# Kernel optimization log

Hardware: AMD Instinct MI355X
Metric: run time of the kernel (lower is better)

Reference implementation:

```python
import jax, jax.numpy as jnp
import numpy as np

B, C2, H, W = 4, 1024, 64, 64  # features have 2*input_dim channels
CH = C2 // 2                   # 512 = input_dim
HID = CH // 4                  # 128 = hidden_channels


def setup_inputs() -> dict:
    key = jax.random.key(0)
    ks = jax.random.split(key, 6)
    left = jax.random.normal(ks[0], (B, C2, H, W), dtype=jnp.float32)
    right = jax.random.normal(ks[1], (B, C2, H, W), dtype=jnp.float32)
    # 1x1 conv params (weight [out,in], bias [out]) for query/reference projections
    Wq = jax.random.normal(ks[2], (HID, CH), dtype=jnp.float32) * 0.02
    bq = jax.random.normal(ks[3], (HID,), dtype=jnp.float32) * 0.02
    Wk = jax.random.normal(ks[4], (HID, CH), dtype=jnp.float32) * 0.02
    bk = jax.random.normal(ks[5], (HID,), dtype=jnp.float32) * 0.02
    return {"left_features": left, "right_features": right, "Wq": Wq, "bq": bq, "Wk": Wk, "bk": bk}


def _co_attention(qf, rf, Wq, bq, Wk, bk):
    # 1x1 convs == per-pixel channel matmuls
    Q = jnp.einsum('bchw,oc->bohw', qf, Wq) + bq[None, :, None, None]   # [B,HID,H,W]
    K = jnp.einsum('bchw,oc->bohw', rf, Wk) + bk[None, :, None, None]   # [B,HID,H,W]
    b, c, h, w = Q.shape
    Kf = K.reshape(b, c, h * w)                                          # [B,HID,P]
    V = rf.reshape(rf.shape[0], rf.shape[1], h * w)                      # [B,CH,P]
    # attention_map: einsum('bcij,bckl->bijkl') then flatten (kl) == contract channels
    attn = jnp.einsum('bcij,bcp->bijp', Q, Kf)                           # [B,H,W,P]
    attn = jax.nn.softmax(attn, axis=3)
    return jnp.einsum('bijp,bcp->bcij', attn, V)                         # [B,CH,H,W]


def _homo(qf, rf):
    weights = jax.nn.softmax(qf - rf, axis=1)  # softmax over channels
    return rf * weights


def _get_both_differences(q, r, Wq, bq, Wk, bk):
    c = q.shape[1] // 2
    q_orig, q_trans = q[:, :c], q[:, c:]
    r_orig = r[:, :c]
    cross = _co_attention(q_orig, r_orig, Wq, bq, Wk, bk)
    reduce = _homo(q_orig, q_trans)
    return jnp.concatenate([q_orig, cross + reduce], axis=1)


def reference(left_features, right_features, Wq, bq, Wk, bk):
    left_out = _get_both_differences(left_features, right_features, Wq, bq, Wk, bk)
    right_out = _get_both_differences(right_features, left_features, Wq, bq, Wk, bk)
    return (left_out, right_out)
```

## Files before the change

kernel.cpp:

```cpp
#include <hip/hip_runtime.h>
#include <hip/hip_bf16.h>

#define NB 4
#define LOG2E 1.4426950408889634f

typedef unsigned short u16;
typedef __attribute__((ext_vector_type(8))) short bf16x8;
typedef __attribute__((ext_vector_type(4))) float f32x4;

static __device__ __forceinline__ float bf2f(u16 u) {
    union { float f; unsigned v; } x; x.v = ((unsigned)u) << 16; return x.f;
}
static __device__ __forceinline__ u16 f2bf(float f) {
    unsigned v = __builtin_bit_cast(unsigned, f);
    return (u16)((v + 0x7FFFu + ((v >> 16) & 1u)) >> 16);
}
static __device__ __forceinline__ void gload_lds16(const u16* g, u16* l) {
    __builtin_amdgcn_global_load_lds(
        (const __attribute__((address_space(1))) unsigned*)(const void*)g,
        (__attribute__((address_space(3))) unsigned*)(void*)l, 16, 0, 0);
}

__global__ void k_wcvt(const float* __restrict__ Wq, const float* __restrict__ Wk,
                       u16* __restrict__ Wbq, u16* __restrict__ Wbk) {
    int i = blockIdx.x * 1024 + threadIdx.x;
    Wbq[i] = f2bf(Wq[i]);
    Wbk[i] = f2bf(Wk[i]);
}

__global__ __launch_bounds__(256) void k_cvtf(
        const float* __restrict__ L, const float* __restrict__ R,
        u16* __restrict__ Lb, u16* __restrict__ Rb,
        u16* __restrict__ web, float* __restrict__ sumsH, float* __restrict__ out) {
    __shared__ float4 red[16][16];
    int idx = blockIdx.x;
    int sb = idx & 7, pblk = (idx >> 3) & 63, cpart = idx >> 9;
    int side = sb & 1, b = sb >> 1;
    int osb = side * 4 + b;
    const float* src = (side ? R : L) + (size_t)b * 1024 * 4096;
    int tid = threadIdx.x;
    int p4 = tid & 15, cg = tid >> 4;
    int p = pblk * 64 + p4 * 4;
    int cbase = cpart * 128 + cg * 8;
    const float* ao = src + (size_t)cbase * 4096 + p;
    const float* at = src + (size_t)(512 + cbase) * 4096 + p;
    u16* lbdst = (side ? Rb : Lb) + ((size_t)b * 512 + cbase) * 4096 + p;
    float* odst = out + ((size_t)osb * 1024 + cbase) * 4096 + p;
    u16* wdst = web + ((size_t)osb * 512 + cbase) * 4096 + p;
    float4 sm = {0.f, 0.f, 0.f, 0.f};
#pragma unroll
    for (int cc = 0; cc < 8; cc++) {
        float4 a = *reinterpret_cast<const float4*>(ao + (size_t)cc * 4096);
        float4 t = *reinterpret_cast<const float4*>(at + (size_t)cc * 4096);
        ushort4 ub;
        ub.x = f2bf(a.x); ub.y = f2bf(a.y); ub.z = f2bf(a.z); ub.w = f2bf(a.w);
        *reinterpret_cast<ushort4*>(lbdst + (size_t)cc * 4096) = ub;
        *reinterpret_cast<float4*>(odst + (size_t)cc * 4096) = a;
        float4 e;
        e.x = exp2f((a.x - t.x) * LOG2E);
        e.y = exp2f((a.y - t.y) * LOG2E);
        e.z = exp2f((a.z - t.z) * LOG2E);
        e.w = exp2f((a.w - t.w) * LOG2E);
        sm.x += e.x; sm.y += e.y; sm.z += e.z; sm.w += e.w;
        ushort4 wb_;
        wb_.x = f2bf(t.x * e.x); wb_.y = f2bf(t.y * e.y);
        wb_.z = f2bf(t.z * e.z); wb_.w = f2bf(t.w * e.w);
        *reinterpret_cast<ushort4*>(wdst + (size_t)cc * 4096) = wb_;
    }
    red[cg][p4] = sm;
    __syncthreads();
    if (tid < 16) {
        float4 tot = {0.f, 0.f, 0.f, 0.f};
#pragma unroll
        for (int gR = 0; gR < 16; gR++) {
            float4 v = red[gR][tid];
            tot.x += v.x; tot.y += v.y; tot.z += v.z; tot.w += v.w;
        }
        *reinterpret_cast<float4*>(
            sumsH + ((size_t)cpart * 8 + osb) * 4096 + pblk * 64 + tid * 4) = tot;
    }
}

__global__ void k_cvt(const float* __restrict__ L, const float* __restrict__ R,
                      u16* __restrict__ Lb, u16* __restrict__ Rb, float* __restrict__ out) {
    int i = blockIdx.x * 256 + threadIdx.x;
    int pq = i & 1023;
    int c = (i >> 10) & 511;
    int b = (i >> 19) & 3;
    int side = i >> 21;
    const float* src = (side ? R : L) + ((long)(b * 1024 + c) << 12) + (pq << 2);
    float4 v = *reinterpret_cast<const float4*>(src);
    ushort4 u;
    u.x = f2bf(v.x); u.y = f2bf(v.y); u.z = f2bf(v.z); u.w = f2bf(v.w);
    *reinterpret_cast<ushort4*>((side ? Rb : Lb) + ((long)(b * 512 + c) << 12) + (pq << 2)) = u;
    *reinterpret_cast<float4*>(out + ((long)(side * 4 + b) * 1024 + c) * 4096 + (pq << 2)) = v;
}

__global__ __launch_bounds__(256) void k_proj(
        const u16* __restrict__ Lb, const u16* __restrict__ Rb,
        const u16* __restrict__ Wbq, const u16* __restrict__ Wbk,
        const float* __restrict__ bq, const float* __restrict__ bk,
        u16* __restrict__ QL, u16* __restrict__ KL,
        u16* __restrict__ QR, u16* __restrict__ KR) {
    __shared__ u16 XT[2][64 * 40];
    int pj = blockIdx.x & 15, pt = blockIdx.x >> 4;
    int ty = pj >> 2, b = pj & 3;
    const u16* src; const u16* Wb; const float* bias; u16* dst;
    if (ty == 0)      { src = Lb; Wb = Wbq; bias = bq; dst = QL; }
    else if (ty == 1) { src = Rb; Wb = Wbk; bias = bk; dst = KL; }
    else if (ty == 2) { src = Rb; Wb = Wbq; bias = bq; dst = QR; }
    else              { src = Lb; Wb = Wbk; bias = bk; dst = KR; }
    const u16* X = src + (long)b * 512 * 4096 + pt * 64;
    int tid = threadIdx.x;
    int wv = __builtin_amdgcn_readfirstlane(tid >> 6);
    int lane = tid & 63, g = lane >> 4, li = lane & 15;

    f32x4 acc[8];
#pragma unroll
    for (int ob = 0; ob < 8; ob++)
#pragma unroll
        for (int r = 0; r < 4; r++) acc[ob][r] = bias[ob * 16 + g * 4 + r];

    int c_r = tid >> 3, j = tid & 7;
    bf16x8 gx = *reinterpret_cast<const bf16x8*>(X + (long)c_r * 4096 + j * 8);
#pragma unroll
    for (int k = 0; k < 8; k++) XT[0][(j * 8 + k) * 40 + c_r] = (u16)gx[k];
    __syncthreads();

    for (int cc = 0; cc < 16; cc++) {
        int buf = cc & 1;
        bf16x8 gn;
        if (cc < 15)
            gn = *reinterpret_cast<const bf16x8*>(X + (long)(cc * 32 + 32 + c_r) * 4096 + j * 8);
        bf16x8 xb = *reinterpret_cast<const bf16x8*>(&XT[buf][(wv * 16 + li) * 40 + g * 8]);
#pragma unroll
        for (int ob = 0; ob < 8; ob++) {
            bf16x8 aw = *reinterpret_cast<const bf16x8*>(Wb + (long)(ob * 16 + li) * 512 + cc * 32 + g * 8);
            acc[ob] = __builtin_amdgcn_mfma_f32_16x16x32_bf16(aw, xb, acc[ob], 0, 0, 0);
        }
        if (cc < 15) {
#pragma unroll
            for (int k = 0; k < 8; k++) XT[buf ^ 1][(j * 8 + k) * 40 + c_r] = (u16)gn[k];
        }
        __syncthreads();
    }
    u16* d = dst + ((long)b * 4096 + pt * 64 + wv * 16 + li) * 128;
#pragma unroll
    for (int ob = 0; ob < 8; ob++) {
        uint2 w;
        w.x = (unsigned)f2bf(acc[ob][0]) | ((unsigned)f2bf(acc[ob][1]) << 16);
        w.y = (unsigned)f2bf(acc[ob][2]) | ((unsigned)f2bf(acc[ob][3]) << 16);
        *reinterpret_cast<uint2*>(d + ob * 16 + g * 4) = w;
    }
}

__global__ __launch_bounds__(512, 4) void k_qk(
        const u16* __restrict__ QL, const u16* __restrict__ KL,
        const u16* __restrict__ QR, const u16* __restrict__ KR,
        u16* __restrict__ P, float* __restrict__ sums,
        int bd0, int bdMask, int bdShift) {
    __shared__ u16 Kl[2][8192];
    __shared__ u16 Ps[4096];
    __shared__ float sred[4][2][16];
    int bdl = (int)blockIdx.x & bdMask;
    int rest = (int)blockIdx.x >> bdShift;
    int qtile = rest & 63;
    int ph0 = rest >> 6;
    int bd = bd0 + bdl, dir = bd & 1, b = bd >> 1;
    const u16* Qt = (dir ? QR : QL) + (size_t)b * 4096 * 128;
    const u16* Kt = (dir ? KR : KL) + (size_t)b * 4096 * 128;
    u16* Pbd = P + ((size_t)bdl << 24);
    int q0 = qtile * 64;
    int tid = threadIdx.x;
    int wv = __builtin_amdgcn_readfirstlane(tid >> 6);
    int lane = tid & 63, g = lane >> 4, li = lane & 15;
    int qt = wv >> 1, phw = wv & 1;

#define STAGE_K(BUF, PT)                                                                   \
    {                                                                                      \
        _Pragma("unroll") for (int r0 = 0; r0 < 2; r0++) {                                 \
            int o = r0 * 8192 + tid * 16;                                                  \
            int row = o >> 8, w = o & 255;                                                 \
            int sw = (w ^ ((row & 7) << 4)) >> 1;                                          \
            gload_lds16(Kt + (((size_t)((PT) * 64 + row)) << 7) + sw,                      \
                        &Kl[BUF][r0 * 4096 + wv * 512]);                                   \
        }                                                                                  \
    }

    bf16x8 qf[4];
#pragma unroll
    for (int hc = 0; hc < 4; hc++)
        qf[hc] = *reinterpret_cast<const bf16x8*>(
            Qt + (size_t)(q0 + qt * 16 + li) * 128 + hc * 32 + g * 8);
    float psum = 0.f;
    STAGE_K(0, ph0 * 32)

    for (int tt = 0; tt < 32; tt++) {
        int pt = ph0 * 32 + tt;
        if (tt == 0) asm volatile("s_waitcnt vmcnt(0) lgkmcnt(0)\n\ts_barrier" ::: "memory");
        else         asm volatile("s_waitcnt vmcnt(1) lgkmcnt(0)\n\ts_barrier" ::: "memory");
        if (tt < 31) STAGE_K((tt + 1) & 1, pt + 1)
        int buf = tt & 1;
        f32x4 sv[2];
        sv[0] = (f32x4){0.f, 0.f, 0.f, 0.f};
        sv[1] = (f32x4){0.f, 0.f, 0.f, 0.f};
        __builtin_amdgcn_s_setprio(1);
#pragma unroll
        for (int ps = 0; ps < 2; ps++) {
            int row = phw * 32 + ps * 16 + li;
            unsigned rb = (unsigned)row * 256;
            unsigned sz = (unsigned)((row & 7) << 4);
#pragma unroll
            for (int hc = 0; hc < 4; hc++) {
                bf16x8 kf = *reinterpret_cast<const bf16x8*>(
                    (char*)Kl[buf] + rb + (((unsigned)(hc * 64 + g * 16)) ^ sz));
                sv[ps] = __builtin_amdgcn_mfma_f32_16x16x32_bf16(kf, qf[hc], sv[ps], 0, 0, 0);
            }
        }
        __builtin_amdgcn_s_setprio(0);
        int qrow = qt * 16 + li;
        unsigned qsz = (unsigned)((qrow & 7) << 4);
#pragma unroll
        for (int ps = 0; ps < 2; ps++) {
            float e0 = exp2f(sv[ps][0] * LOG2E);
            float e1 = exp2f(sv[ps][1] * LOG2E);
            float e2 = exp2f(sv[ps][2] * LOG2E);
            float e3 = exp2f(sv[ps][3] * LOG2E);
            psum += (e0 + e1) + (e2 + e3);
            uint2 pk;
            pk.x = (unsigned)f2bf(e0) | ((unsigned)f2bf(e1) << 16);
            pk.y = (unsigned)f2bf(e2) | ((unsigned)f2bf(e3) << 16);
            unsigned off = (unsigned)qrow * 128 +
                           (((unsigned)(phw * 64 + ps * 32 + g * 8)) ^ qsz);
            *reinterpret_cast<uint2*>((char*)Ps + off) = pk;
        }
        asm volatile("s_waitcnt lgkmcnt(0)\n\ts_barrier" ::: "memory");
        {
            uint4 d = *reinterpret_cast<const uint4*>((char*)Ps + tid * 16);
            *reinterpret_cast<uint4*>(
                Pbd + ((size_t)(qtile * 64 + pt) << 12) + tid * 8) = d;
        }
    }
    psum += __shfl_xor(psum, 16);
    psum += __shfl_xor(psum, 32);
    if (lane < 16) sred[qt][phw][li] = psum;
    __syncthreads();
    if (phw == 0 && lane < 16) {
        float s = sred[qt][0][li] + sred[qt][1][li];
        sums[((size_t)ph0 * 8 + bd) * 4096 + q0 + qt * 16 + li] = s;
    }
#undef STAGE_K
}

template<int FUSEH>
__global__ __launch_bounds__(256, 2) void k_pv(
        const u16* __restrict__ Lb, const u16* __restrict__ Rb,
        const u16* __restrict__ P, const float* __restrict__ sums,
        const u16* __restrict__ web, const float* __restrict__ sumsH,
        float* __restrict__ out, int bd0, int bdMask, int bdShift) {
    __shared__ u16 Tl[2][2][8192];
    int bdl = (int)blockIdx.x & bdMask;
    int idx = (int)blockIdx.x >> bdShift;
    int mtile = idx & 3;
    int ntile = idx >> 2;
    int bd = bd0 + bdl, dir = bd & 1, b = bd >> 1;
    int osb = dir * 4 + b;
    const u16* V = (dir ? Lb : Rb) + (size_t)b * 512 * 4096;
    const u16* Pbd = P + ((size_t)bdl << 24);
    int q0 = ntile * 128, c0 = mtile * 128, qt0 = ntile * 2;
    int tid = threadIdx.x;
    int wv = __builtin_amdgcn_readfirstlane(tid >> 6);
    int lane = tid & 63, g = lane >> 4, li = lane & 15;
    int wr = wv >> 1, wc = wv & 1;

#define STAGE_PV(BUF, T)                                                                   \
    {                                                                                      \
        _Pragma("unroll") for (int r0 = 0; r0 < 4; r0++) {                                 \
            int o = r0 * 4096 + tid * 16;                                                  \
            int row = o >> 7, w = o & 127;                                                 \
            int sw = (w ^ ((row & 7) << 4)) >> 1;                                          \
            gload_lds16(V + (((size_t)(c0 + row)) << 12) + (T) * 64 + sw,                  \
                        &Tl[BUF][0][r0 * 2048 + wv * 512]);                                \
            gload_lds16(Pbd + (((size_t)((qt0 + (r0 >> 1)) * 64 + (T))) << 12) +           \
                            (r0 & 1) * 2048 + tid * 8,                                     \
                        &Tl[BUF][1][r0 * 2048 + wv * 512]);                                \
        }                                                                                  \
    }

    f32x4 acc[4][4];
#pragma unroll
    for (int i = 0; i < 4; i++)
#pragma unroll
        for (int j = 0; j < 4; j++) acc[i][j] = (f32x4){0.f, 0.f, 0.f, 0.f};

    STAGE_PV(0, 0)

    for (int t = 0; t < 64; t++) {
        asm volatile("s_waitcnt vmcnt(0) lgkmcnt(0)\n\ts_barrier" ::: "memory");
        if (t < 63) STAGE_PV((t + 1) & 1, t + 1)
        int buf = t & 1;
        bf16x8 af[4][2], bf[4][2];
#pragma unroll
        for (int mi = 0; mi < 4; mi++) {
            int row = wr * 64 + mi * 16 + li;
            unsigned rb = (unsigned)row * 128, sz = (unsigned)((row & 7) << 4);
#pragma unroll
            for (int kk = 0; kk < 2; kk++)
                af[mi][kk] = *reinterpret_cast<const bf16x8*>(
                    (char*)Tl[buf][0] + rb + (((unsigned)(kk * 64 + g * 16)) ^ sz));
        }
#pragma unroll
        for (int ni = 0; ni < 4; ni++) {
            int row = wc * 64 + ni * 16 + li;
            unsigned rb = (unsigned)row * 128, sz = (unsigned)((row & 7) << 4);
#pragma unroll
            for (int kk = 0; kk < 2; kk++)
                bf[ni][kk] = *reinterpret_cast<const bf16x8*>(
                    (char*)Tl[buf][1] + rb + (((unsigned)(kk * 64 + g * 16)) ^ sz));
        }
        __builtin_amdgcn_s_setprio(1);
#pragma unroll
        for (int kk = 0; kk < 2; kk++)
#pragma unroll
            for (int mi = 0; mi < 4; mi++)
#pragma unroll
                for (int ni = 0; ni < 4; ni++)
                    acc[mi][ni] = __builtin_amdgcn_mfma_f32_16x16x32_bf16(
                        af[mi][kk], bf[ni][kk], acc[mi][ni], 0, 0, 0);
        __builtin_amdgcn_s_setprio(0);
    }

    float* obase = out + ((size_t)osb * 1024 + 512) * 4096;
    const u16* wb = web + (size_t)osb * 512 * 4096;
#pragma unroll
    for (int ni = 0; ni < 4; ni++) {
        int q = q0 + wc * 64 + ni * 16 + li;
        float s0 = sums[(size_t)bd * 4096 + q];
        float s1 = sums[((size_t)8 + bd) * 4096 + q];
        float linv = 1.0f / (s0 + s1);
        float hinv = 0.f;
        if (FUSEH) {
            float hs = sumsH[(size_t)osb * 4096 + q] +
                       sumsH[((size_t)8 + osb) * 4096 + q] +
                       sumsH[((size_t)16 + osb) * 4096 + q] +
                       sumsH[((size_t)24 + osb) * 4096 + q];
            hinv = 1.0f / hs;
        }
#pragma unroll
        for (int mi = 0; mi < 4; mi++) {
            int c = c0 + wr * 64 + mi * 16 + g * 4;
#pragma unroll
            for (int r = 0; r < 4; r++) {
                float v = acc[mi][ni][r] * linv;
                if (FUSEH) v += bf2f(wb[(size_t)(c + r) * 4096 + q]) * hinv;
                obase[(size_t)(c + r) * 4096 + q] = v;
            }
        }
    }
#undef STAGE_PV
}

__global__ __launch_bounds__(256) void k_homo(const float* __restrict__ L,
                                              const float* __restrict__ R,
                                              float* __restrict__ out) {
    __shared__ float4 red[16][16];
    int sb = blockIdx.x & 7, pblk = blockIdx.x >> 3;
    int side = sb & 1, b = sb >> 1;
    const float* src = (side ? R : L) + (long)b * 1024 * 4096;
    float* o = out + (long)(side * 4 + b) * 1024 * 4096;
    int p4 = threadIdx.x & 15, cg = threadIdx.x >> 4;
    int p = pblk * 64 + p4 * 4;
    const float* qo = src + p;
    const float* qt = src + (long)512 * 4096 + p;
    float4 sm = {0.f, 0.f, 0.f, 0.f};
    for (int c = cg * 32; c < cg * 32 + 32; c++) {
        float4 a = *reinterpret_cast<const float4*>(qo + (long)c * 4096);
        float4 t = *reinterpret_cast<const float4*>(qt + (long)c * 4096);
        sm.x += exp2f((a.x - t.x) * LOG2E);
        sm.y += exp2f((a.y - t.y) * LOG2E);
        sm.z += exp2f((a.z - t.z) * LOG2E);
        sm.w += exp2f((a.w - t.w) * LOG2E);
    }
    red[cg][p4] = sm;
    __syncthreads();
    float4 tot = {0.f, 0.f, 0.f, 0.f};
#pragma unroll
    for (int gR = 0; gR < 16; gR++) {
        float4 v = red[gR][p4];
        tot.x += v.x; tot.y += v.y; tot.z += v.z; tot.w += v.w;
    }
    float4 rinv = {1.0f / tot.x, 1.0f / tot.y, 1.0f / tot.z, 1.0f / tot.w};
    for (int c = cg * 32; c < cg * 32 + 32; c++) {
        float4 a = *reinterpret_cast<const float4*>(qo + (long)c * 4096);
        float4 t = *reinterpret_cast<const float4*>(qt + (long)c * 4096);
        float4* op = reinterpret_cast<float4*>(o + (long)(512 + c) * 4096 + p);
        float4 cur = *op;
        cur.x += t.x * exp2f((a.x - t.x) * LOG2E) * rinv.x;
        cur.y += t.y * exp2f((a.y - t.y) * LOG2E) * rinv.y;
        cur.z += t.z * exp2f((a.z - t.z) * LOG2E) * rinv.z;
        cur.w += t.w * exp2f((a.w - t.w) * LOG2E) * rinv.w;
        *op = cur;
    }
}

extern "C" void kernel_launch(void* const* d_in, const int* in_sizes, int n_in,
                              void* d_out, int out_size, void* d_ws, size_t ws_size,
                              hipStream_t stream) {
    const float* L  = (const float*)d_in[0];
    const float* R  = (const float*)d_in[1];
    const float* Wq = (const float*)d_in[2];
    const float* bq = (const float*)d_in[3];
    const float* Wk = (const float*)d_in[4];
    const float* bk = (const float*)d_in[5];
    float* out = (float*)d_out;
    char* ws = (char*)d_ws;

    size_t off = 0;
    u16* Wbq = (u16*)(ws + off); off += (size_t)128 * 512 * 2;
    u16* Wbk = (u16*)(ws + off); off += (size_t)128 * 512 * 2;
    u16* QL = (u16*)(ws + off); off += (size_t)NB * 4096 * 128 * 2;
    u16* KL = (u16*)(ws + off); off += (size_t)NB * 4096 * 128 * 2;
    u16* QR = (u16*)(ws + off); off += (size_t)NB * 4096 * 128 * 2;
    u16* KR = (u16*)(ws + off); off += (size_t)NB * 4096 * 128 * 2;
    u16* Lb = (u16*)(ws + off); off += (size_t)NB * 512 * 4096 * 2;
    u16* Rb = (u16*)(ws + off); off += (size_t)NB * 512 * 4096 * 2;
    float* sums = (float*)(ws + off); off += (size_t)2 * 8 * 4096 * 4;
    float* sumsH = (float*)(ws + off); off += (size_t)4 * 8 * 4096 * 4;
    size_t off_nofuse = off;
    u16* web = (u16*)(ws + off); off += (size_t)8 * 512 * 4096 * 2;
    off = (off + 255) & ~(size_t)255;
    size_t pchunk4 = (size_t)4 * 4096 * 4096 * 2;
    size_t pchunk1 = (size_t)4096 * 4096 * 2;

    k_wcvt <<<64, 1024, 0, stream>>>(Wq, Wk, Wbq, Wbk);

    if (ws_size >= off + pchunk4) {
        u16* Pb = (u16*)(ws + off);
        k_cvtf <<<2048, 256, 0, stream>>>(L, R, Lb, Rb, web, sumsH, out);
        k_proj <<<1024, 256, 0, stream>>>(Lb, Rb, Wbq, Wbk, bq, bk, QL, KL, QR, KR);
        for (int c = 0; c < 2; c++) {
            k_qk    <<<512, 512, 0, stream>>>(QL, KL, QR, KR, Pb, sums, c * 4, 3, 2);
            k_pv<1> <<<512, 256, 0, stream>>>(Lb, Rb, Pb, sums, web, sumsH, out, c * 4, 3, 2);
        }
    } else {
        int nbd, bdShift;
        size_t poff = (off_nofuse + 255) & ~(size_t)255;
        if (ws_size >= poff + pchunk4) { nbd = 4; bdShift = 2; }
        else                           { nbd = 1; bdShift = 0; }
        int bdMask = nbd - 1, nchunk = 8 / nbd;
        u16* Pb = (u16*)(ws + poff);
        k_cvt  <<<16384, 256, 0, stream>>>(L, R, Lb, Rb, out);
        k_proj <<<1024,  256, 0, stream>>>(Lb, Rb, Wbq, Wbk, bq, bk, QL, KL, QR, KR);
        for (int c = 0; c < nchunk; c++) {
            k_qk    <<<nbd * 128, 512, 0, stream>>>(QL, KL, QR, KR, Pb, sums,
                                                    c * nbd, bdMask, bdShift);
            k_pv<0> <<<nbd * 128, 256, 0, stream>>>(Lb, Rb, Pb, sums, web, sumsH, out,
                                                    c * nbd, bdMask, bdShift);
        }
        k_homo <<<512, 256, 0, stream>>>(L, R, out);
    }
}
```

Before: 404.6 us.

## Triple-buffer K and PV staging; restructure homo-sum reduction with separate hsum kernel

The QK and PV kernels move from double-buffered to triple-buffered LDS staging, prefetching two tiles ahead with relaxed vmcnt waits, so global loads have more time to overlap MFMA work. Launch bounds drop occupancy to fit the larger shared buffers. The fused conversion kernel now has each block span 1024 pixels and 8 channels, writing 64 partial channel sums. A new small kernel reduces these into reciprocal softmax denominators, so the PV epilogue reads one value instead of summing four. The trade-off is lower occupancy and an extra launch plus a larger partial-sum buffer.

```diff
diff --git a/kernel.cpp b/kernel.cpp
--- a/kernel.cpp
+++ b/kernel.cpp
@@ -32,53 +32,68 @@
         const float* __restrict__ L, const float* __restrict__ R,
         u16* __restrict__ Lb, u16* __restrict__ Rb,
         u16* __restrict__ web, float* __restrict__ sumsH, float* __restrict__ out) {
-    __shared__ float4 red[16][16];
+    __shared__ float pred[4][1024];
     int idx = blockIdx.x;
-    int sb = idx & 7, pblk = (idx >> 3) & 63, cpart = idx >> 9;
+    int sb = idx & 7, pseg = (idx >> 3) & 3, cpart = idx >> 5;
     int side = sb & 1, b = sb >> 1;
     int osb = side * 4 + b;
     const float* src = (side ? R : L) + (size_t)b * 1024 * 4096;
-    int tid = threadIdx.x;
-    int p4 = tid & 15, cg = tid >> 4;
-    int p = pblk * 64 + p4 * 4;
-    int cbase = cpart * 128 + cg * 8;
-    const float* ao = src + (size_t)cbase * 4096 + p;
-    const float* at = src + (size_t)(512 + cbase) * 4096 + p;
-    u16* lbdst = (side ? Rb : Lb) + ((size_t)b * 512 + cbase) * 4096 + p;
-    float* odst = out + ((size_t)osb * 1024 + cbase) * 4096 + p;
-    u16* wdst = web + ((size_t)osb * 512 + cbase) * 4096 + p;
-    float4 sm = {0.f, 0.f, 0.f, 0.f};
-#pragma unroll
-    for (int cc = 0; cc < 8; cc++) {
-        float4 a = *reinterpret_cast<const float4*>(ao + (size_t)cc * 4096);
-        float4 t = *reinterpret_cast<const float4*>(at + (size_t)cc * 4096);
-        ushort4 ub;
-        ub.x = f2bf(a.x); ub.y = f2bf(a.y); ub.z = f2bf(a.z); ub.w = f2bf(a.w);
-        *reinterpret_cast<ushort4*>(lbdst + (size_t)cc * 4096) = ub;
-        *reinterpret_cast<float4*>(odst + (size_t)cc * 4096) = a;
-        float4 e;
-        e.x = exp2f((a.x - t.x) * LOG2E);
-        e.y = exp2f((a.y - t.y) * LOG2E);
-        e.z = exp2f((a.z - t.z) * LOG2E);
-        e.w = exp2f((a.w - t.w) * LOG2E);
-        sm.x += e.x; sm.y += e.y; sm.z += e.z; sm.w += e.w;
-        ushort4 wb_;
-        wb_.x = f2bf(t.x * e.x); wb_.y = f2bf(t.y * e.y);
-        wb_.z = f2bf(t.z * e.z); wb_.w = f2bf(t.w * e.w);
-        *reinterpret_cast<ushort4*>(wdst + (size_t)cc * 4096) = wb_;
-    }
-    red[cg][p4] = sm;
+    u16* lbbase = (side ? Rb : Lb) + (size_t)b * 512 * 4096;
+    int tid = threadIdx.x, wv = tid >> 6, lane = tid & 63;
+    int p0 = pseg * 1024;
+    int cA = cpart * 8 + wv * 2;
+#pragma unroll
+    for (int s = 0; s < 4; s++) {
+        int p = p0 + s * 256 + lane * 4;
+        float4 sm = {0.f, 0.f, 0.f, 0.f};
+#pragma unroll
+        for (int cc = 0; cc < 2; cc++) {
+            int c = cA + cc;
+            float4 a = *reinterpret_cast<const float4*>(src + (size_t)c * 4096 + p);
+            float4 t = *reinterpret_cast<const float4*>(src + (size_t)(512 + c) * 4096 + p);
+            ushort4 ub;
+            ub.x = f2bf(a.x); ub.y = f2bf(a.y); ub.z = f2bf(a.z); ub.w = f2bf(a.w);
+            *reinterpret_cast<ushort4*>(lbbase + (size_t)c * 4096 + p) = ub;
+            *reinterpret_cast<float4*>(out + ((size_t)osb * 1024 + c) * 4096 + p) = a;
+            float4 e;
+            e.x = exp2f((a.x - t.x) * LOG2E);
+            e.y = exp2f((a.y - t.y) * LOG2E);
+            e.z = exp2f((a.z - t.z) * LOG2E);
+            e.w = exp2f((a.w - t.w) * LOG2E);
+            sm.x += e.x; sm.y += e.y; sm.z += e.z; sm.w += e.w;
+            ushort4 wb_;
+            wb_.x = f2bf(t.x * e.x); wb_.y = f2bf(t.y * e.y);
+            wb_.z = f2bf(t.z * e.z); wb_.w = f2bf(t.w * e.w);
+            *reinterpret_cast<ushort4*>(web + ((size_t)osb * 512 + c) * 4096 + p) = wb_;
+        }
+        *reinterpret_cast<float4*>(&pred[wv][s * 256 + lane * 4]) = sm;
+    }
     __syncthreads();
-    if (tid < 16) {
-        float4 tot = {0.f, 0.f, 0.f, 0.f};
-#pragma unroll
-        for (int gR = 0; gR < 16; gR++) {
-            float4 v = red[gR][tid];
-            tot.x += v.x; tot.y += v.y; tot.z += v.z; tot.w += v.w;
-        }
+    {
+        float4 t0 = *reinterpret_cast<const float4*>(&pred[0][tid * 4]);
+        float4 t1 = *reinterpret_cast<const float4*>(&pred[1][tid * 4]);
+        float4 t2 = *reinterpret_cast<const float4*>(&pred[2][tid * 4]);
+        float4 t3 = *reinterpret_cast<const float4*>(&pred[3][tid * 4]);
+        float4 tot;
+        tot.x = (t0.x + t1.x) + (t2.x + t3.x);
+        tot.y = (t0.y + t1.y) + (t2.y + t3.y);
+        tot.z = (t0.z + t1.z) + (t2.z + t3.z);
+        tot.w = (t0.w + t1.w) + (t2.w + t3.w);
         *reinterpret_cast<float4*>(
-            sumsH + ((size_t)cpart * 8 + osb) * 4096 + pblk * 64 + tid * 4) = tot;
-    }
+            sumsH + ((size_t)cpart * 8 + osb) * 4096 + p0 + tid * 4) = tot;
+    }
+}
+
+__global__ __launch_bounds__(256) void k_hsum(const float* __restrict__ sumsH,
+                                              float* __restrict__ hinv) {
+    int i = blockIdx.x * 256 + threadIdx.x;
+    float4 tot = {0.f, 0.f, 0.f, 0.f};
+    for (int cp = 0; cp < 64; cp++) {
+        float4 v = *reinterpret_cast<const float4*>(sumsH + (size_t)cp * 8 * 4096 + (size_t)i * 4);
+        tot.x += v.x; tot.y += v.y; tot.z += v.z; tot.w += v.w;
+    }
+    float4 r = {1.0f / tot.x, 1.0f / tot.y, 1.0f / tot.z, 1.0f / tot.w};
+    *reinterpret_cast<float4*>(hinv + (size_t)i * 4) = r;
 }
 
 __global__ void k_cvt(const float* __restrict__ L, const float* __restrict__ R,
@@ -154,12 +169,12 @@
     }
 }
 
-__global__ __launch_bounds__(512, 4) void k_qk(
+__global__ __launch_bounds__(512, 2) void k_qk(
         const u16* __restrict__ QL, const u16* __restrict__ KL,
         const u16* __restrict__ QR, const u16* __restrict__ KR,
         u16* __restrict__ P, float* __restrict__ sums,
         int bd0, int bdMask, int bdShift) {
-    __shared__ u16 Kl[2][8192];
+    __shared__ u16 Kl[3][8192];
     __shared__ u16 Ps[4096];
     __shared__ float sred[4][2][16];
     int bdl = (int)blockIdx.x & bdMask;
@@ -194,13 +209,19 @@
             Qt + (size_t)(q0 + qt * 16 + li) * 128 + hc * 32 + g * 8);
     float psum = 0.f;
     STAGE_K(0, ph0 * 32)
-
+    STAGE_K(1, ph0 * 32 + 1)
+
+    int cur = 0;
     for (int tt = 0; tt < 32; tt++) {
         int pt = ph0 * 32 + tt;
-        if (tt == 0) asm volatile("s_waitcnt vmcnt(0) lgkmcnt(0)\n\ts_barrier" ::: "memory");
-        else         asm volatile("s_waitcnt vmcnt(1) lgkmcnt(0)\n\ts_barrier" ::: "memory");
-        if (tt < 31) STAGE_K((tt + 1) & 1, pt + 1)
-        int buf = tt & 1;
+        if (tt == 0)       asm volatile("s_waitcnt vmcnt(2) lgkmcnt(0)\n\ts_barrier" ::: "memory");
+        else if (tt == 1)  asm volatile("s_waitcnt vmcnt(3) lgkmcnt(0)\n\ts_barrier" ::: "memory");
+        else if (tt == 31) asm volatile("s_waitcnt vmcnt(2) lgkmcnt(0)\n\ts_barrier" ::: "memory");
+        else               asm volatile("s_waitcnt vmcnt(4) lgkmcnt(0)\n\ts_barrier" ::: "memory");
+        if (tt < 30) {
+            int stg = cur + 2; if (stg >= 3) stg -= 3;
+            STAGE_K(stg, pt + 2)
+        }
         f32x4 sv[2];
         sv[0] = (f32x4){0.f, 0.f, 0.f, 0.f};
         sv[1] = (f32x4){0.f, 0.f, 0.f, 0.f};
@@ -213,7 +234,7 @@
 #pragma unroll
             for (int hc = 0; hc < 4; hc++) {
                 bf16x8 kf = *reinterpret_cast<const bf16x8*>(
-                    (char*)Kl[buf] + rb + (((unsigned)(hc * 64 + g * 16)) ^ sz));
+                    (char*)Kl[cur] + rb + (((unsigned)(hc * 64 + g * 16)) ^ sz));
                 sv[ps] = __builtin_amdgcn_mfma_f32_16x16x32_bf16(kf, qf[hc], sv[ps], 0, 0, 0);
             }
         }
@@ -240,6 +261,7 @@
             *reinterpret_cast<uint4*>(
                 Pbd + ((size_t)(qtile * 64 + pt) << 12) + tid * 8) = d;
         }
+        cur = (cur + 1 == 3) ? 0 : cur + 1;
     }
     psum += __shfl_xor(psum, 16);
     psum += __shfl_xor(psum, 32);
@@ -253,12 +275,12 @@
 }
 
 template<int FUSEH>
-__global__ __launch_bounds__(256, 2) void k_pv(
+__global__ __launch_bounds__(256, 1) void k_pv(
         const u16* __restrict__ Lb, const u16* __restrict__ Rb,
         const u16* __restrict__ P, const float* __restrict__ sums,
-        const u16* __restrict__ web, const float* __restrict__ sumsH,
+        const u16* __restrict__ web, const float* __restrict__ hinvArr,
         float* __restrict__ out, int bd0, int bdMask, int bdShift) {
-    __shared__ u16 Tl[2][2][8192];
+    __shared__ u16 Tl[3][2][8192];
     int bdl = (int)blockIdx.x & bdMask;
     int idx = (int)blockIdx.x >> bdShift;
     int mtile = idx & 3;
@@ -294,11 +316,16 @@
         for (int j = 0; j < 4; j++) acc[i][j] = (f32x4){0.f, 0.f, 0.f, 0.f};
 
     STAGE_PV(0, 0)
-
+    STAGE_PV(1, 1)
+
+    int cur = 0;
     for (int t = 0; t < 64; t++) {
-        asm volatile("s_waitcnt vmcnt(0) lgkmcnt(0)\n\ts_barrier" ::: "memory");
-        if (t < 63) STAGE_PV((t + 1) & 1, t + 1)
-        int buf = t & 1;
+        if (t < 63) asm volatile("s_waitcnt vmcnt(8) lgkmcnt(0)\n\ts_barrier" ::: "memory");
+        else        asm volatile("s_waitcnt vmcnt(0) lgkmcnt(0)\n\ts_barrier" ::: "memory");
+        if (t < 62) {
+            int stg = cur + 2; if (stg >= 3) stg -= 3;
+            STAGE_PV(stg, t + 2)
+        }
         bf16x8 af[4][2], bf[4][2];
 #pragma unroll
         for (int mi = 0; mi < 4; mi++) {
@@ -307,7 +334,7 @@
 #pragma unroll
             for (int kk = 0; kk < 2; kk++)
                 af[mi][kk] = *reinterpret_cast<const bf16x8*>(
-                    (char*)Tl[buf][0] + rb + (((unsigned)(kk * 64 + g * 16)) ^ sz));
+                    (char*)Tl[cur][0] + rb + (((unsigned)(kk * 64 + g * 16)) ^ sz));
         }
 #pragma unroll
         for (int ni = 0; ni < 4; ni++) {
@@ -316,7 +343,7 @@
 #pragma unroll
             for (int kk = 0; kk < 2; kk++)
                 bf[ni][kk] = *reinterpret_cast<const bf16x8*>(
-                    (char*)Tl[buf][1] + rb + (((unsigned)(kk * 64 + g * 16)) ^ sz));
+                    (char*)Tl[cur][1] + rb + (((unsigned)(kk * 64 + g * 16)) ^ sz));
         }
         __builtin_amdgcn_s_setprio(1);
 #pragma unroll
@@ -328,6 +355,7 @@
                     acc[mi][ni] = __builtin_amdgcn_mfma_f32_16x16x32_bf16(
                         af[mi][kk], bf[ni][kk], acc[mi][ni], 0, 0, 0);
         __builtin_amdgcn_s_setprio(0);
+        cur = (cur + 1 == 3) ? 0 : cur + 1;
     }
 
     float* obase = out + ((size_t)osb * 1024 + 512) * 4096;
@@ -339,13 +367,7 @@
         float s1 = sums[((size_t)8 + bd) * 4096 + q];
         float linv = 1.0f / (s0 + s1);
         float hinv = 0.f;
-        if (FUSEH) {
-            float hs = sumsH[(size_t)osb * 4096 + q] +
-                       sumsH[((size_t)8 + osb) * 4096 + q] +
-                       sumsH[((size_t)16 + osb) * 4096 + q] +
-                       sumsH[((size_t)24 + osb) * 4096 + q];
-            hinv = 1.0f / hs;
-        }
+        if (FUSEH) hinv = hinvArr[(size_t)osb * 4096 + q];
 #pragma unroll
         for (int mi = 0; mi < 4; mi++) {
             int c = c0 + wr * 64 + mi * 16 + g * 4;
@@ -425,22 +447,23 @@
     u16* Lb = (u16*)(ws + off); off += (size_t)NB * 512 * 4096 * 2;
     u16* Rb = (u16*)(ws + off); off += (size_t)NB * 512 * 4096 * 2;
     float* sums = (float*)(ws + off); off += (size_t)2 * 8 * 4096 * 4;
-    float* sumsH = (float*)(ws + off); off += (size_t)4 * 8 * 4096 * 4;
+    float* hinv = (float*)(ws + off); off += (size_t)8 * 4096 * 4;
     size_t off_nofuse = off;
+    float* sumsH = (float*)(ws + off); off += (size_t)64 * 8 * 4096 * 4;
     u16* web = (u16*)(ws + off); off += (size_t)8 * 512 * 4096 * 2;
     off = (off + 255) & ~(size_t)255;
     size_t pchunk4 = (size_t)4 * 4096 * 4096 * 2;
-    size_t pchunk1 = (size_t)4096 * 4096 * 2;
 
     k_wcvt <<<64, 1024, 0, stream>>>(Wq, Wk, Wbq, Wbk);
 
     if (ws_size >= off + pchunk4) {
         u16* Pb = (u16*)(ws + off);
         k_cvtf <<<2048, 256, 0, stream>>>(L, R, Lb, Rb, web, sumsH, out);
+        k_hsum <<<32,   256, 0, stream>>>(sumsH, hinv);
         k_proj <<<1024, 256, 0, stream>>>(Lb, Rb, Wbq, Wbk, bq, bk, QL, KL, QR, KR);
         for (int c = 0; c < 2; c++) {
             k_qk    <<<512, 512, 0, stream>>>(QL, KL, QR, KR, Pb, sums, c * 4, 3, 2);
-            k_pv<1> <<<512, 256, 0, stream>>>(Lb, Rb, Pb, sums, web, sumsH, out, c * 4, 3, 2);
+            k_pv<1> <<<512, 256, 0, stream>>>(Lb, Rb, Pb, sums, web, hinv, out, c * 4, 3, 2);
         }
     } else {
         int nbd, bdShift;
@@ -454,7 +477,7 @@
         for (int c = 0; c < nchunk; c++) {
             k_qk    <<<nbd * 128, 512, 0, stream>>>(QL, KL, QR, KR, Pb, sums,
                                                     c * nbd, bdMask, bdShift);
-            k_pv<0> <<<nbd * 128, 256, 0, stream>>>(Lb, Rb, Pb, sums, web, sumsH, out,
+            k_pv<0> <<<nbd * 128, 256, 0, stream>>>(Lb, Rb, Pb, sums, web, hinv, out,
                                                     c * nbd, bdMask, bdShift);
         }
         k_homo <<<512, 256, 0, stream>>>(L, R, out);
```

Result: slower. 461.2 us (+14.0%).
